# Kernel optimization log

Hardware: AMD Instinct MI355X
Metric: run time of the kernel (lower is better)

Reference implementation:

```python
import jax, jax.numpy as jnp
import numpy as np

TOP_K = 2  # num_expert in the torch module


def setup_inputs() -> dict:
    key = jax.random.key(0)
    ks = jax.random.split(key, 8)
    B, C, H, W, E, Dh = 8, 512, 32, 32, 8, 1024
    inputs = jax.random.normal(ks[0], (B, C, H, W), dtype=jnp.float32)
    k = jax.random.uniform(ks[1], (B, 1, 1, 1), dtype=jnp.float32)
    # gate: global-avg-pool + Linear(C -> E)
    Wg = jax.random.normal(ks[2], (C, E), dtype=jnp.float32) / np.sqrt(C)
    bg = jnp.zeros((E,), dtype=jnp.float32)
    # experts: per-expert 2-layer channel MLP (1x1-conv style), modulated by k
    W1 = jax.random.normal(ks[3], (E, C, Dh), dtype=jnp.float32) / np.sqrt(C)
    b1 = jnp.zeros((E, Dh), dtype=jnp.float32)
    W2 = jax.random.normal(ks[4], (E, Dh, C), dtype=jnp.float32) / np.sqrt(Dh)
    b2 = jnp.zeros((E, C), dtype=jnp.float32)
    return {"inputs": inputs, "k": k, "Wg": Wg, "bg": bg,
            "W1": W1, "b1": b1, "W2": W2, "b2": b2}


def reference(inputs, k, Wg, bg, W1, b1, W2, b2):
    B = inputs.shape[0]
    # --- gate: softmax in fp32, cast back (matches F.softmax(dtype=torch.float)) ---
    logits = jnp.mean(inputs, axis=(2, 3)) @ Wg + bg            # [B, E]
    weights = jax.nn.softmax(logits.astype(jnp.float32), axis=1).astype(inputs.dtype)
    topk_w, topk_idx = jax.lax.top_k(weights, TOP_K)            # [B, K]
    # --- scatter top-k gate weights into dense [B, E] mask (training path) ---
    exp_w = jnp.zeros_like(weights).at[jnp.arange(B)[:, None], topk_idx].set(topk_w)
    # --- run ALL experts densely (training-mode math), masked combine ---
    h = jnp.einsum('bchw,ecd->bedhw', inputs, W1) + b1[None, :, :, None, None]
    h = jax.nn.gelu(h, approximate=False)                        # [B,E,Dh,H,W]
    y = jnp.einsum('bedhw,edc->bechw', h, W2) + b2[None, :, :, None, None]
    y = y * k[:, None]                                           # per-sample scalar mod
    out = inputs + jnp.einsum('bechw,be->bchw', y, exp_w)        # residual + weighted sum
    return out
```

## Files before the change

kernel.cpp:

```cpp
#include <hip/hip_runtime.h>
#include <hip/hip_bf16.h>
#include <math.h>


typedef __bf16 bf16_t;
typedef __attribute__((ext_vector_type(8))) __bf16 bf16x8;
typedef __attribute__((ext_vector_type(4))) __bf16 bf16x4;
typedef __attribute__((ext_vector_type(4))) float f32x4;

#define GLDS(g, l) __builtin_amdgcn_global_load_lds(                      \
    (const __attribute__((address_space(1))) void*)(const void*)(g),       \
    (__attribute__((address_space(3))) void*)(void*)(l), 16, 0, 0)

__device__ __forceinline__ float gelu_fast(float x) {
    float z = x * 0.70710678118654752f;
    float az = fabsf(z);
    float t = 1.0f / (1.0f + 0.3275911f * az);
    float p = ((((1.061405429f * t - 1.453152027f) * t + 1.421413741f) * t
                - 0.284496736f) * t + 0.254829592f) * t;
    float e = __expf(-az * az);
    float er = copysignf(1.0f - p * e, z);
    return 0.5f * x * (1.0f + er);
}

__global__ void transpose_cvt_all(const float* __restrict__ x, const float* __restrict__ W1,
                                  const float* __restrict__ W2, bf16_t* __restrict__ xT,
                                  bf16_t* __restrict__ W1t, bf16_t* __restrict__ W2t,
                                  float* __restrict__ msum) {
    int id = blockIdx.x;
    const float* src; bf16_t* dst; int R, Cols, csh; bool dm = false;
    if (id < 4096)      { src = x;  dst = xT;  R = 512;  Cols = 1024; csh = 5; dm = true; }
    else if (id < 8192) { id -= 4096; src = W1; dst = W1t; R = 512;  Cols = 1024; csh = 5; }
    else                { id -= 8192; src = W2; dst = W2t; R = 1024; Cols = 512; csh = 4; }
    const int bz = id >> 9, t = id & 511;
    const int c0 = (t & ((1 << csh) - 1)) * 32, r0 = (t >> csh) * 32;
    const float* s = src + (size_t)bz * R * Cols;
    bf16_t* d = dst + (size_t)bz * R * Cols;
    __shared__ float tile[32][33];
    const int tid = threadIdx.x;
    const int lr = tid >> 3, lc = (tid & 7) * 4;
    float4 v = *(const float4*)(s + (size_t)(r0 + lr) * Cols + c0 + lc);
    tile[lr][lc + 0] = v.x; tile[lr][lc + 1] = v.y;
    tile[lr][lc + 2] = v.z; tile[lr][lc + 3] = v.w;
    if (dm) {
        float ps = v.x + v.y + v.z + v.w;
        ps += __shfl_down(ps, 4, 8);
        ps += __shfl_down(ps, 2, 8);
        ps += __shfl_down(ps, 1, 8);
        if ((tid & 7) == 0) atomicAdd(&msum[bz * 512 + r0 + lr], ps);
    }
    __syncthreads();
    bf16x4 o = { (bf16_t)tile[lc + 0][lr], (bf16_t)tile[lc + 1][lr],
                 (bf16_t)tile[lc + 2][lr], (bf16_t)tile[lc + 3][lr] };
    *(bf16x4*)(d + (size_t)(c0 + lr) * R + r0 + lc) = o;
}

__global__ void gate_kernel(const float* __restrict__ msum, const float* __restrict__ Wg,
                            const float* __restrict__ bg, const float* __restrict__ kmod,
                            int* __restrict__ tidx, float* __restrict__ scale) {
    const int tid = threadIdx.x;
    const int b = tid >> 6, l = tid & 63;
    float a[8] = {0.f, 0.f, 0.f, 0.f, 0.f, 0.f, 0.f, 0.f};
    for (int c = l; c < 512; c += 64) {
        float m = msum[b * 512 + c];
        #pragma unroll
        for (int e = 0; e < 8; ++e) a[e] += m * Wg[c * 8 + e];
    }
    #pragma unroll
    for (int e = 0; e < 8; ++e)
        #pragma unroll
        for (int off = 32; off; off >>= 1) a[e] += __shfl_xor(a[e], off, 64);
    if (l == 0) {
        float lg[8], mx = -1e30f;
        #pragma unroll
        for (int e = 0; e < 8; ++e) { lg[e] = a[e] * (1.0f / 1024.0f) + bg[e]; mx = fmaxf(mx, lg[e]); }
        float sum = 0.f;
        #pragma unroll
        for (int e = 0; e < 8; ++e) { lg[e] = expf(lg[e] - mx); sum += lg[e]; }
        float inv = 1.0f / sum;
        float best = -1.f; int i0 = 0;
        for (int j = 0; j < 8; ++j) { float w = lg[j] * inv; if (w > best) { best = w; i0 = j; } }
        float best2 = -1.f; int i1 = 0;
        for (int j = 0; j < 8; ++j) { if (j == i0) continue; float w = lg[j] * inv; if (w > best2) { best2 = w; i1 = j; } }
        float kb = kmod[b];
        tidx[b * 2] = i0; tidx[b * 2 + 1] = i1;
        scale[b * 2] = best * kb; scale[b * 2 + 1] = best2 * kb;
    }
}

__global__ __launch_bounds__(256, 4) void gemm1_kernel(
    const bf16_t* __restrict__ W1t, const bf16_t* __restrict__ xT,
    const float* __restrict__ b1, const int* __restrict__ tidx,
    const float* __restrict__ scale, bf16_t* __restrict__ hT) {
    __shared__ bf16_t smem[16384];
    const int bid = blockIdx.x;
    const int pair = bid >> 6, rem = bid & 63;
    const int b = pair >> 1, slot = pair & 1;
    const int e = tidx[pair];
    const float s = scale[pair];
    const int d0 = (rem >> 3) * 128, n0 = (rem & 7) * 128;
    const int tid = threadIdx.x;
    const int lane = tid & 63, wave = tid >> 6;
    const int wm = (wave & 1) * 64, wn = (wave >> 1) * 64;
    const int lrow = lane & 15, quad = lane >> 4;

    const bf16_t* gA = W1t + (size_t)e * 524288 + (size_t)d0 * 512;
    const bf16_t* gB = xT + (size_t)b * 524288 + (size_t)n0 * 512;
    const int r0s = tid >> 2, kcs = (tid & 3) * 8;
    f32x4 acc[4][4];
    #pragma unroll
    for (int i = 0; i < 4; ++i)
        #pragma unroll
        for (int j = 0; j < 4; ++j) acc[i][j] = (f32x4){0.f, 0.f, 0.f, 0.f};

    GLDS(gA + r0s * 512 + kcs, smem + tid * 8);
    GLDS(gA + (64 + r0s) * 512 + kcs, smem + (256 + tid) * 8);
    GLDS(gB + r0s * 512 + kcs, smem + 8192 + tid * 8);
    GLDS(gB + (64 + r0s) * 512 + kcs, smem + 8192 + (256 + tid) * 8);
    __syncthreads();

    for (int it = 0; it < 16; ++it) {
        const int cur = it & 1;
        if (it < 15) {
            const int kn = (it + 1) * 32;
            bf16_t* dA = smem + (cur ^ 1) * 4096;
            bf16_t* dB = smem + 8192 + (cur ^ 1) * 4096;
            GLDS(gA + r0s * 512 + kn + kcs, dA + tid * 8);
            GLDS(gA + (64 + r0s) * 512 + kn + kcs, dA + (256 + tid) * 8);
            GLDS(gB + r0s * 512 + kn + kcs, dB + tid * 8);
            GLDS(gB + (64 + r0s) * 512 + kn + kcs, dB + (256 + tid) * 8);
        }
        const bf16_t* cA = smem + cur * 4096;
        const bf16_t* cB = smem + 8192 + cur * 4096;
        bf16x8 af[4], bfr[4];
        #pragma unroll
        for (int i = 0; i < 4; ++i) {
            af[i] = *(const bf16x8*)&cA[(wm + i * 16 + lrow) * 32 + quad * 8];
            bfr[i] = *(const bf16x8*)&cB[(wn + i * 16 + lrow) * 32 + quad * 8];
        }
        #pragma unroll
        for (int i = 0; i < 4; ++i)
            #pragma unroll
            for (int j = 0; j < 4; ++j)
                acc[i][j] = __builtin_amdgcn_mfma_f32_16x16x32_bf16(af[i], bfr[j], acc[i][j], 0, 0, 0);
        __syncthreads();
    }

    bf16_t* hTb = hT + (size_t)b * 2097152 + slot * 1024;
    float4 bb[4];
    #pragma unroll
    for (int i = 0; i < 4; ++i)
        bb[i] = *(const float4*)(b1 + e * 1024 + d0 + wm + i * 16 + quad * 4);

    for (int half = 0; half < 2; ++half) {
        if (wn == half * 64) {
            #pragma unroll
            for (int i = 0; i < 4; ++i)
                #pragma unroll
                for (int j = 0; j < 4; ++j) {
                    const int hw_l = j * 16 + lrow;
                    const int d_l = wm + i * 16 + quad * 4;
                    f32x4 a = acc[i][j];
                    bf16x4 o = { (bf16_t)(gelu_fast(a[0] + bb[i].x) * s),
                                 (bf16_t)(gelu_fast(a[1] + bb[i].y) * s),
                                 (bf16_t)(gelu_fast(a[2] + bb[i].z) * s),
                                 (bf16_t)(gelu_fast(a[3] + bb[i].w) * s) };
                    *(bf16x4*)&smem[hw_l * 136 + d_l] = o;
                }
        }
        __syncthreads();
        #pragma unroll
        for (int q = 0; q < 4; ++q) {
            const int cid = q * 256 + tid;
            const int row = cid >> 4, c16 = cid & 15;
            bf16x8 v = *(const bf16x8*)&smem[row * 136 + c16 * 8];
            *(bf16x8*)(hTb + (size_t)(n0 + half * 64 + row) * 2048 + d0 + c16 * 8) = v;
        }
        __syncthreads();
    }
}

__global__ __launch_bounds__(256, 5) void gemm2_kernel(
    const bf16_t* __restrict__ W2t, const bf16_t* __restrict__ hT,
    const float* __restrict__ b2, const int* __restrict__ tidx,
    const float* __restrict__ scale, const float* __restrict__ x,
    float* __restrict__ out) {
    __shared__ bf16_t smem[16384];
    const int bid = blockIdx.x;
    const int b = bid >> 7, rem = bid & 127;
    const int c0 = (rem >> 4) * 64, n0 = (rem & 15) * 64;
    const int e0 = tidx[b * 2], e1 = tidx[b * 2 + 1];
    const float s0 = scale[b * 2], s1 = scale[b * 2 + 1];
    const int tid = threadIdx.x;
    const int lane = tid & 63, wave = tid >> 6;
    const int wm = (wave & 1) * 32, wn = (wave >> 1) * 32;
    const int lrow = lane & 15, quad = lane >> 4;

    const bf16_t* hTb = hT + (size_t)b * 2097152 + (size_t)n0 * 2048;
    const bf16_t* A0 = W2t + (size_t)e0 * 524288 + (size_t)c0 * 1024;
    const bf16_t* A1 = W2t + (size_t)e1 * 524288 + (size_t)c0 * 1024;
    const int sr = tid >> 2, kcs = (tid & 3) * 8;

    f32x4 acc[2][2];
    #pragma unroll
    for (int i = 0; i < 2; ++i)
        #pragma unroll
        for (int j = 0; j < 2; ++j) acc[i][j] = (f32x4){0.f, 0.f, 0.f, 0.f};

    auto stage = [&](int st, int it) {
        const int k0 = it * 64;
        const bf16_t* gA = ((k0 < 1024) ? A0 : A1) + (size_t)sr * 1024 + (k0 & 1023);
        bf16_t* dA = smem + st * 4096;
        bf16_t* dB = smem + 8192 + st * 4096;
        GLDS(gA + kcs, dA + tid * 8);
        GLDS(gA + 32 + kcs, dA + 2048 + tid * 8);
        const bf16_t* gBp = hTb + (size_t)sr * 2048 + k0;
        GLDS(gBp + kcs, dB + tid * 8);
        GLDS(gBp + 32 + kcs, dB + 2048 + tid * 8);
    };

    stage(0, 0);
    __syncthreads();

    for (int it = 0; it < 32; ++it) {
        const int cur = it & 1;
        if (it < 31) stage(cur ^ 1, it + 1);
        const bf16_t* cA = smem + cur * 4096;
        const bf16_t* cB = smem + 8192 + cur * 4096;
        #pragma unroll
        for (int ks = 0; ks < 2; ++ks) {
            bf16x8 af[2], bfr[2];
            #pragma unroll
            for (int i = 0; i < 2; ++i) {
                af[i] = *(const bf16x8*)&cA[ks * 2048 + (wm + i * 16 + lrow) * 32 + quad * 8];
                bfr[i] = *(const bf16x8*)&cB[ks * 2048 + (wn + i * 16 + lrow) * 32 + quad * 8];
            }
            #pragma unroll
            for (int i = 0; i < 2; ++i)
                #pragma unroll
                for (int j = 0; j < 2; ++j)
                    acc[i][j] = __builtin_amdgcn_mfma_f32_16x16x32_bf16(af[i], bfr[j], acc[i][j], 0, 0, 0);
        }
        __syncthreads();
    }

    #pragma unroll
    for (int i = 0; i < 2; ++i) {
        const int c_l = c0 + wm + i * 16 + quad * 4;
        const float4 bA = *(const float4*)(b2 + e0 * 512 + c_l);
        const float4 bB = *(const float4*)(b2 + e1 * 512 + c_l);
        const float bias[4] = { s0 * bA.x + s1 * bB.x, s0 * bA.y + s1 * bB.y,
                                s0 * bA.z + s1 * bB.z, s0 * bA.w + s1 * bB.w };
        #pragma unroll
        for (int j = 0; j < 2; ++j) {
            const int hw = n0 + wn + j * 16 + lrow;
            #pragma unroll
            for (int r = 0; r < 4; ++r) {
                const size_t o = (size_t)(b * 512 + c_l + r) * 1024 + hw;
                out[o] = x[o] + acc[i][j][r] + bias[r];
            }
        }
    }
}

extern "C" void kernel_launch(void* const* d_in, const int* in_sizes, int n_in,
                              void* d_out, int out_size, void* d_ws, size_t ws_size,
                              hipStream_t stream) {
    const float* x    = (const float*)d_in[0];
    const float* kmod = (const float*)d_in[1];
    const float* Wg   = (const float*)d_in[2];
    const float* bg   = (const float*)d_in[3];
    const float* W1   = (const float*)d_in[4];
    const float* b1   = (const float*)d_in[5];
    const float* W2   = (const float*)d_in[6];
    const float* b2   = (const float*)d_in[7];
    float* out = (float*)d_out;

    char* ws = (char*)d_ws;
    float* msum = (float*)ws;
    float* scl  = (float*)(ws + 16384);
    int*   tix  = (int*)(ws + 16448);
    bf16_t* xT  = (bf16_t*)(ws + 32768);
    bf16_t* W1t = (bf16_t*)(ws + 32768 + (size_t)8388608);
    bf16_t* W2t = (bf16_t*)(ws + 32768 + (size_t)2 * 8388608);
    bf16_t* hT  = (bf16_t*)(ws + 32768 + (size_t)3 * 8388608);

    hipMemsetAsync(msum, 0, 8 * 512 * sizeof(float), stream);
    transpose_cvt_all<<<12288, 256, 0, stream>>>(x, W1, W2, xT, W1t, W2t, msum);
    gate_kernel<<<1, 512, 0, stream>>>(msum, Wg, bg, kmod, tix, scl);
    gemm1_kernel<<<1024, 256, 0, stream>>>(W1t, xT, b1, tix, scl, hT);
    gemm2_kernel<<<1024, 256, 0, stream>>>(W2t, hT, b2, tix, scl, x, out);
}
```

Baseline: 177.9 us.

## Enlarge GEMM and transpose tiles, replace atomic mean with partial sums

The transpose kernel moves to 64x64 tiles and writes per-tile partial row sums into scratch, which replaces the memset and atomicAdd path. The gate kernel now reduces those partials. GEMM1 tiles grow to 128x256 per block and GEMM2 tiles to 128x128 with a K=64 stage, which raises data reuse per block and cuts the number of blocks. The trade-off is more registers and LDS per block, lower occupancy, and fewer blocks to spread across the CUs (256 for GEMM2).

```diff
diff --git a/kernel.cpp b/kernel.cpp
--- a/kernel.cpp
+++ b/kernel.cpp
@@ -23,46 +23,56 @@
     return 0.5f * x * (1.0f + er);
 }
 
-__global__ void transpose_cvt_all(const float* __restrict__ x, const float* __restrict__ W1,
-                                  const float* __restrict__ W2, bf16_t* __restrict__ xT,
-                                  bf16_t* __restrict__ W1t, bf16_t* __restrict__ W2t,
-                                  float* __restrict__ msum) {
+__global__ __launch_bounds__(256) void transpose_cvt_all(
+    const float* __restrict__ x, const float* __restrict__ W1,
+    const float* __restrict__ W2, bf16_t* __restrict__ xT,
+    bf16_t* __restrict__ W1t, bf16_t* __restrict__ W2t, float* __restrict__ pp) {
     int id = blockIdx.x;
-    const float* src; bf16_t* dst; int R, Cols, csh; bool dm = false;
-    if (id < 4096)      { src = x;  dst = xT;  R = 512;  Cols = 1024; csh = 5; dm = true; }
-    else if (id < 8192) { id -= 4096; src = W1; dst = W1t; R = 512;  Cols = 1024; csh = 5; }
-    else                { id -= 8192; src = W2; dst = W2t; R = 1024; Cols = 512; csh = 4; }
-    const int bz = id >> 9, t = id & 511;
-    const int c0 = (t & ((1 << csh) - 1)) * 32, r0 = (t >> csh) * 32;
-    const float* s = src + (size_t)bz * R * Cols;
-    bf16_t* d = dst + (size_t)bz * R * Cols;
-    __shared__ float tile[32][33];
+    const float* src; bf16_t* dst; int Rows, Cols, csh; bool dm = false;
+    if (id < 1024)      { src = x;  dst = xT;  Rows = 512;  Cols = 1024; csh = 4; dm = true; }
+    else if (id < 2048) { id -= 1024; src = W1; dst = W1t; Rows = 512;  Cols = 1024; csh = 4; }
+    else                { id -= 2048; src = W2; dst = W2t; Rows = 1024; Cols = 512; csh = 3; }
+    const int bz = id >> 7, t = id & 127;
+    const int ct = t & ((1 << csh) - 1), rt = t >> csh;
+    const int r0 = rt * 64, c0 = ct * 64;
+    __shared__ float tile[64][65];
     const int tid = threadIdx.x;
-    const int lr = tid >> 3, lc = (tid & 7) * 4;
-    float4 v = *(const float4*)(s + (size_t)(r0 + lr) * Cols + c0 + lc);
-    tile[lr][lc + 0] = v.x; tile[lr][lc + 1] = v.y;
-    tile[lr][lc + 2] = v.z; tile[lr][lc + 3] = v.w;
+    const int lr = tid >> 2, ch = tid & 3;
+    const float* srow = src + (size_t)bz * Rows * Cols + (size_t)(r0 + lr) * Cols + c0 + ch * 16;
+    float4 v0 = ((const float4*)srow)[0];
+    float4 v1 = ((const float4*)srow)[1];
+    float4 v2 = ((const float4*)srow)[2];
+    float4 v3 = ((const float4*)srow)[3];
+    float* trow = &tile[lr][ch * 16];
+    *(float4*)(trow + 0) = v0; *(float4*)(trow + 4) = v1;
+    *(float4*)(trow + 8) = v2; *(float4*)(trow + 12) = v3;
     if (dm) {
-        float ps = v.x + v.y + v.z + v.w;
-        ps += __shfl_down(ps, 4, 8);
-        ps += __shfl_down(ps, 2, 8);
-        ps += __shfl_down(ps, 1, 8);
-        if ((tid & 7) == 0) atomicAdd(&msum[bz * 512 + r0 + lr], ps);
+        float s = v0.x + v0.y + v0.z + v0.w + v1.x + v1.y + v1.z + v1.w
+                + v2.x + v2.y + v2.z + v2.w + v3.x + v3.y + v3.z + v3.w;
+        s += __shfl_down(s, 2, 4);
+        s += __shfl_down(s, 1, 4);
+        if (ch == 0) pp[(bz * 16 + ct) * 512 + r0 + lr] = s;
     }
     __syncthreads();
-    bf16x4 o = { (bf16_t)tile[lc + 0][lr], (bf16_t)tile[lc + 1][lr],
-                 (bf16_t)tile[lc + 2][lr], (bf16_t)tile[lc + 3][lr] };
-    *(bf16x4*)(d + (size_t)(c0 + lr) * R + r0 + lc) = o;
-}
-
-__global__ void gate_kernel(const float* __restrict__ msum, const float* __restrict__ Wg,
+    const int oc = tid >> 2;
+    bf16_t ov[16];
+    #pragma unroll
+    for (int j = 0; j < 16; ++j) ov[j] = (bf16_t)tile[ch * 16 + j][oc];
+    bf16_t* drow = dst + (size_t)bz * Rows * Cols + (size_t)(c0 + oc) * Rows + r0 + ch * 16;
+    *(bf16x8*)(drow + 0) = *(bf16x8*)&ov[0];
+    *(bf16x8*)(drow + 8) = *(bf16x8*)&ov[8];
+}
+
+__global__ void gate_kernel(const float* __restrict__ pp, const float* __restrict__ Wg,
                             const float* __restrict__ bg, const float* __restrict__ kmod,
                             int* __restrict__ tidx, float* __restrict__ scale) {
     const int tid = threadIdx.x;
     const int b = tid >> 6, l = tid & 63;
     float a[8] = {0.f, 0.f, 0.f, 0.f, 0.f, 0.f, 0.f, 0.f};
     for (int c = l; c < 512; c += 64) {
-        float m = msum[b * 512 + c];
+        float m = 0.f;
+        #pragma unroll
+        for (int ht = 0; ht < 16; ++ht) m += pp[(b * 16 + ht) * 512 + c];
         #pragma unroll
         for (int e = 0; e < 8; ++e) a[e] += m * Wg[c * 8 + e];
     }
@@ -88,60 +98,61 @@
     }
 }
 
-__global__ __launch_bounds__(256, 4) void gemm1_kernel(
+__global__ __launch_bounds__(256, 2) void gemm1_kernel(
     const bf16_t* __restrict__ W1t, const bf16_t* __restrict__ xT,
     const float* __restrict__ b1, const int* __restrict__ tidx,
     const float* __restrict__ scale, bf16_t* __restrict__ hT) {
-    __shared__ bf16_t smem[16384];
+    __shared__ bf16_t smem[24576];
     const int bid = blockIdx.x;
-    const int pair = bid >> 6, rem = bid & 63;
+    const int pair = bid >> 5, rem = bid & 31;
     const int b = pair >> 1, slot = pair & 1;
     const int e = tidx[pair];
     const float s = scale[pair];
-    const int d0 = (rem >> 3) * 128, n0 = (rem & 7) * 128;
+    const int d0 = (rem >> 2) * 128, n0 = (rem & 3) * 256;
     const int tid = threadIdx.x;
     const int lane = tid & 63, wave = tid >> 6;
-    const int wm = (wave & 1) * 64, wn = (wave >> 1) * 64;
+    const int wm = (wave & 1) * 64, wn = (wave >> 1) * 128;
     const int lrow = lane & 15, quad = lane >> 4;
 
     const bf16_t* gA = W1t + (size_t)e * 524288 + (size_t)d0 * 512;
     const bf16_t* gB = xT + (size_t)b * 524288 + (size_t)n0 * 512;
-    const int r0s = tid >> 2, kcs = (tid & 3) * 8;
-    f32x4 acc[4][4];
+    const int r2 = tid >> 2, kc = (tid & 3) * 8;
+
+    f32x4 acc[4][8];
     #pragma unroll
     for (int i = 0; i < 4; ++i)
         #pragma unroll
-        for (int j = 0; j < 4; ++j) acc[i][j] = (f32x4){0.f, 0.f, 0.f, 0.f};
-
-    GLDS(gA + r0s * 512 + kcs, smem + tid * 8);
-    GLDS(gA + (64 + r0s) * 512 + kcs, smem + (256 + tid) * 8);
-    GLDS(gB + r0s * 512 + kcs, smem + 8192 + tid * 8);
-    GLDS(gB + (64 + r0s) * 512 + kcs, smem + 8192 + (256 + tid) * 8);
+        for (int j = 0; j < 8; ++j) acc[i][j] = (f32x4){0.f, 0.f, 0.f, 0.f};
+
+    auto stage = [&](int st, int k0) {
+        bf16_t* dA = smem + st * 4096;
+        bf16_t* dB = smem + 8192 + st * 8192;
+        GLDS(gA + (size_t)r2 * 512 + k0 + kc, dA + tid * 8);
+        GLDS(gA + (size_t)(64 + r2) * 512 + k0 + kc, dA + (256 + tid) * 8);
+        #pragma unroll
+        for (int p = 0; p < 4; ++p)
+            GLDS(gB + (size_t)(p * 64 + r2) * 512 + k0 + kc, dB + (p * 256 + tid) * 8);
+    };
+
+    stage(0, 0);
     __syncthreads();
 
     for (int it = 0; it < 16; ++it) {
         const int cur = it & 1;
-        if (it < 15) {
-            const int kn = (it + 1) * 32;
-            bf16_t* dA = smem + (cur ^ 1) * 4096;
-            bf16_t* dB = smem + 8192 + (cur ^ 1) * 4096;
-            GLDS(gA + r0s * 512 + kn + kcs, dA + tid * 8);
-            GLDS(gA + (64 + r0s) * 512 + kn + kcs, dA + (256 + tid) * 8);
-            GLDS(gB + r0s * 512 + kn + kcs, dB + tid * 8);
-            GLDS(gB + (64 + r0s) * 512 + kn + kcs, dB + (256 + tid) * 8);
-        }
+        if (it < 15) stage(cur ^ 1, (it + 1) * 32);
         const bf16_t* cA = smem + cur * 4096;
-        const bf16_t* cB = smem + 8192 + cur * 4096;
-        bf16x8 af[4], bfr[4];
-        #pragma unroll
-        for (int i = 0; i < 4; ++i) {
+        const bf16_t* cB = smem + 8192 + cur * 8192;
+        bf16x8 af[4], bfr[8];
+        #pragma unroll
+        for (int i = 0; i < 4; ++i)
             af[i] = *(const bf16x8*)&cA[(wm + i * 16 + lrow) * 32 + quad * 8];
-            bfr[i] = *(const bf16x8*)&cB[(wn + i * 16 + lrow) * 32 + quad * 8];
-        }
+        #pragma unroll
+        for (int j = 0; j < 8; ++j)
+            bfr[j] = *(const bf16x8*)&cB[(wn + j * 16 + lrow) * 32 + quad * 8];
         #pragma unroll
         for (int i = 0; i < 4; ++i)
             #pragma unroll
-            for (int j = 0; j < 4; ++j)
+            for (int j = 0; j < 8; ++j)
                 acc[i][j] = __builtin_amdgcn_mfma_f32_16x16x32_bf16(af[i], bfr[j], acc[i][j], 0, 0, 0);
         __syncthreads();
     }
@@ -152,13 +163,14 @@
     for (int i = 0; i < 4; ++i)
         bb[i] = *(const float4*)(b1 + e * 1024 + d0 + wm + i * 16 + quad * 4);
 
-    for (int half = 0; half < 2; ++half) {
-        if (wn == half * 64) {
+    for (int chk = 0; chk < 4; ++chk) {
+        if ((wn >> 7) == (chk >> 1)) {
             #pragma unroll
             for (int i = 0; i < 4; ++i)
                 #pragma unroll
-                for (int j = 0; j < 4; ++j) {
-                    const int hw_l = j * 16 + lrow;
+                for (int jj = 0; jj < 4; ++jj) {
+                    const int j = (chk & 1) * 4 + jj;
+                    const int hw_l = jj * 16 + lrow;
                     const int d_l = wm + i * 16 + quad * 4;
                     f32x4 a = acc[i][j];
                     bf16x4 o = { (bf16_t)(gelu_fast(a[0] + bb[i].x) * s),
@@ -171,52 +183,53 @@
         __syncthreads();
         #pragma unroll
         for (int q = 0; q < 4; ++q) {
-            const int cid = q * 256 + tid;
-            const int row = cid >> 4, c16 = cid & 15;
+            const int idx = q * 256 + tid;
+            const int row = idx >> 4, c16 = idx & 15;
             bf16x8 v = *(const bf16x8*)&smem[row * 136 + c16 * 8];
-            *(bf16x8*)(hTb + (size_t)(n0 + half * 64 + row) * 2048 + d0 + c16 * 8) = v;
+            *(bf16x8*)(hTb + (size_t)(n0 + chk * 64 + row) * 2048 + d0 + c16 * 8) = v;
         }
         __syncthreads();
     }
 }
 
-__global__ __launch_bounds__(256, 5) void gemm2_kernel(
+__global__ __launch_bounds__(256) void gemm2_kernel(
     const bf16_t* __restrict__ W2t, const bf16_t* __restrict__ hT,
     const float* __restrict__ b2, const int* __restrict__ tidx,
     const float* __restrict__ scale, const float* __restrict__ x,
     float* __restrict__ out) {
-    __shared__ bf16_t smem[16384];
+    __shared__ bf16_t smem[32768];
     const int bid = blockIdx.x;
-    const int b = bid >> 7, rem = bid & 127;
-    const int c0 = (rem >> 4) * 64, n0 = (rem & 15) * 64;
+    const int b = bid >> 5, rem = bid & 31;
+    const int c0 = (rem >> 3) * 128, n0 = (rem & 7) * 128;
     const int e0 = tidx[b * 2], e1 = tidx[b * 2 + 1];
     const float s0 = scale[b * 2], s1 = scale[b * 2 + 1];
     const int tid = threadIdx.x;
     const int lane = tid & 63, wave = tid >> 6;
-    const int wm = (wave & 1) * 32, wn = (wave >> 1) * 32;
+    const int wm = (wave & 1) * 64, wn = (wave >> 1) * 64;
     const int lrow = lane & 15, quad = lane >> 4;
 
     const bf16_t* hTb = hT + (size_t)b * 2097152 + (size_t)n0 * 2048;
     const bf16_t* A0 = W2t + (size_t)e0 * 524288 + (size_t)c0 * 1024;
     const bf16_t* A1 = W2t + (size_t)e1 * 524288 + (size_t)c0 * 1024;
-    const int sr = tid >> 2, kcs = (tid & 3) * 8;
-
-    f32x4 acc[2][2];
-    #pragma unroll
-    for (int i = 0; i < 2; ++i)
-        #pragma unroll
-        for (int j = 0; j < 2; ++j) acc[i][j] = (f32x4){0.f, 0.f, 0.f, 0.f};
+    const int r3 = tid >> 3, kc2 = (tid & 7) * 8;
+
+    f32x4 acc[4][4];
+    #pragma unroll
+    for (int i = 0; i < 4; ++i)
+        #pragma unroll
+        for (int j = 0; j < 4; ++j) acc[i][j] = (f32x4){0.f, 0.f, 0.f, 0.f};
 
     auto stage = [&](int st, int it) {
         const int k0 = it * 64;
-        const bf16_t* gA = ((k0 < 1024) ? A0 : A1) + (size_t)sr * 1024 + (k0 & 1023);
-        bf16_t* dA = smem + st * 4096;
-        bf16_t* dB = smem + 8192 + st * 4096;
-        GLDS(gA + kcs, dA + tid * 8);
-        GLDS(gA + 32 + kcs, dA + 2048 + tid * 8);
-        const bf16_t* gBp = hTb + (size_t)sr * 2048 + k0;
-        GLDS(gBp + kcs, dB + tid * 8);
-        GLDS(gBp + 32 + kcs, dB + 2048 + tid * 8);
+        const bf16_t* gA = ((k0 < 1024) ? A0 : A1) + (size_t)r3 * 1024 + (k0 & 1023);
+        const bf16_t* gB = hTb + (size_t)r3 * 2048 + k0;
+        bf16_t* dA = smem + st * 8192;
+        bf16_t* dB = smem + 16384 + st * 8192;
+        #pragma unroll
+        for (int p = 0; p < 4; ++p) {
+            GLDS(gA + (size_t)(p * 32) * 1024 + kc2, dA + (p * 256 + tid) * 8);
+            GLDS(gB + (size_t)(p * 32) * 2048 + kc2, dB + (p * 256 + tid) * 8);
+        }
     };
 
     stage(0, 0);
@@ -225,34 +238,34 @@
     for (int it = 0; it < 32; ++it) {
         const int cur = it & 1;
         if (it < 31) stage(cur ^ 1, it + 1);
-        const bf16_t* cA = smem + cur * 4096;
-        const bf16_t* cB = smem + 8192 + cur * 4096;
-        #pragma unroll
-        for (int ks = 0; ks < 2; ++ks) {
-            bf16x8 af[2], bfr[2];
-            #pragma unroll
-            for (int i = 0; i < 2; ++i) {
-                af[i] = *(const bf16x8*)&cA[ks * 2048 + (wm + i * 16 + lrow) * 32 + quad * 8];
-                bfr[i] = *(const bf16x8*)&cB[ks * 2048 + (wn + i * 16 + lrow) * 32 + quad * 8];
+        const bf16_t* cA = smem + cur * 8192;
+        const bf16_t* cB = smem + 16384 + cur * 8192;
+        #pragma unroll
+        for (int kh = 0; kh < 2; ++kh) {
+            bf16x8 af[4], bfr[4];
+            #pragma unroll
+            for (int i = 0; i < 4; ++i) {
+                af[i] = *(const bf16x8*)&cA[(wm + i * 16 + lrow) * 64 + kh * 32 + quad * 8];
+                bfr[i] = *(const bf16x8*)&cB[(wn + i * 16 + lrow) * 64 + kh * 32 + quad * 8];
             }
             #pragma unroll
-            for (int i = 0; i < 2; ++i)
+            for (int i = 0; i < 4; ++i)
                 #pragma unroll
-                for (int j = 0; j < 2; ++j)
+                for (int j = 0; j < 4; ++j)
                     acc[i][j] = __builtin_amdgcn_mfma_f32_16x16x32_bf16(af[i], bfr[j], acc[i][j], 0, 0, 0);
         }
         __syncthreads();
     }
 
     #pragma unroll
-    for (int i = 0; i < 2; ++i) {
+    for (int i = 0; i < 4; ++i) {
         const int c_l = c0 + wm + i * 16 + quad * 4;
         const float4 bA = *(const float4*)(b2 + e0 * 512 + c_l);
         const float4 bB = *(const float4*)(b2 + e1 * 512 + c_l);
         const float bias[4] = { s0 * bA.x + s1 * bB.x, s0 * bA.y + s1 * bB.y,
                                 s0 * bA.z + s1 * bB.z, s0 * bA.w + s1 * bB.w };
         #pragma unroll
-        for (int j = 0; j < 2; ++j) {
+        for (int j = 0; j < 4; ++j) {
             const int hw = n0 + wn + j * 16 + lrow;
             #pragma unroll
             for (int r = 0; r < 4; ++r) {
@@ -277,17 +290,16 @@
     float* out = (float*)d_out;
 
     char* ws = (char*)d_ws;
-    float* msum = (float*)ws;
-    float* scl  = (float*)(ws + 16384);
-    int*   tix  = (int*)(ws + 16448);
+    int*   tix  = (int*)ws;
+    float* scl  = (float*)(ws + 64);
     bf16_t* xT  = (bf16_t*)(ws + 32768);
     bf16_t* W1t = (bf16_t*)(ws + 32768 + (size_t)8388608);
     bf16_t* W2t = (bf16_t*)(ws + 32768 + (size_t)2 * 8388608);
     bf16_t* hT  = (bf16_t*)(ws + 32768 + (size_t)3 * 8388608);
-
-    hipMemsetAsync(msum, 0, 8 * 512 * sizeof(float), stream);
-    transpose_cvt_all<<<12288, 256, 0, stream>>>(x, W1, W2, xT, W1t, W2t, msum);
-    gate_kernel<<<1, 512, 0, stream>>>(msum, Wg, bg, kmod, tix, scl);
-    gemm1_kernel<<<1024, 256, 0, stream>>>(W1t, xT, b1, tix, scl, hT);
-    gemm2_kernel<<<1024, 256, 0, stream>>>(W2t, hT, b2, tix, scl, x, out);
-}
+    float* pp   = (float*)hT;
+
+    transpose_cvt_all<<<3072, 256, 0, stream>>>(x, W1, W2, xT, W1t, W2t, pp);
+    gate_kernel<<<1, 512, 0, stream>>>(pp, Wg, bg, kmod, tix, scl);
+    gemm1_kernel<<<512, 256, 0, stream>>>(W1t, xT, b1, tix, scl, hT);
+    gemm2_kernel<<<256, 256, 0, stream>>>(W2t, hT, b2, tix, scl, x, out);
+}
```

Measured after the change: 344.5 us. +93.6%, slower.
